# Optimization experiments

Measured on AMD Instinct MI355X. Metric: run time of the kernel, lower is better.

## Reference

```python
import jax, jax.numpy as jnp
import numpy as np

K = 2048  # num_embeddings
D = 64    # embedding_dim


def setup_inputs() -> dict:
    key = jax.random.key(0)
    k1, k2 = jax.random.split(key)
    inputs = jax.random.normal(k1, (64, 32, 32, D), dtype=jnp.float32)
    # tf.random_uniform_initializer default: U[0, 1)
    embeddings = jax.random.uniform(k2, (K, D), dtype=jnp.float32)
    return {"inputs": inputs, "embeddings": embeddings}


def reference(inputs, embeddings):
    input_shape = inputs.shape
    flat_inputs = inputs.reshape(-1, D)  # [N, D]
    distances = (
        jnp.sum(flat_inputs ** 2, axis=1, keepdims=True)
        - 2.0 * jnp.matmul(flat_inputs, embeddings.T)
        + jnp.sum(embeddings ** 2, axis=1)
    )
    encoding_indices = jnp.argmin(distances, axis=1)  # [N]
    quantized = embeddings[encoding_indices].reshape(input_shape)
    # straight-through estimator
    quantized = inputs + jax.lax.stop_gradient(quantized - inputs)
    return quantized, encoding_indices, flat_inputs
```

## Files before the change

### kernel.cpp

```cpp
#include <hip/hip_runtime.h>
#include <cfloat>

#define N_TOTAL 65536
#define DIM     64
#define NEMB    2048

typedef __attribute__((ext_vector_type(8))) _Float16 half8;
typedef __attribute__((ext_vector_type(4))) float    floatx4;

__global__ void prep_kernel(const float* __restrict__ emb,
                            half8* __restrict__ ehp, float* __restrict__ en) {
    const int t = blockIdx.x * 256 + threadIdx.x;
    {
        const int l   = t & 63;
        const int ks  = (t >> 6) & 1;
        const int g   = t >> 7;
        const int col = g * 16 + (l & 15);
        const int kb  = ks * 32 + (l >> 4) * 8;
        const float* s = emb + col * DIM + kb;
        float4 v0 = *(const float4*)s, v1 = *(const float4*)(s + 4);
        half8 hv;
        hv[0] = (_Float16)v0.x; hv[1] = (_Float16)v0.y;
        hv[2] = (_Float16)v0.z; hv[3] = (_Float16)v0.w;
        hv[4] = (_Float16)v1.x; hv[5] = (_Float16)v1.y;
        hv[6] = (_Float16)v1.z; hv[7] = (_Float16)v1.w;
        ehp[t] = hv;
    }
    if (t < NEMB * 4) {
        const int row = t >> 2, seg = t & 3;
        const float* s = emb + row * DIM + seg * 16;
        float acc = 0.f;
#pragma unroll
        for (int i = 0; i < 4; ++i) {
            float4 v = ((const float4*)s)[i];
            acc = fmaf(v.x, v.x, acc); acc = fmaf(v.y, v.y, acc);
            acc = fmaf(v.z, v.z, acc); acc = fmaf(v.w, v.w, acc);
        }
        acc += __shfl_xor(acc, 1, 64);
        acc += __shfl_xor(acc, 2, 64);
        if (seg == 0) en[row] = acc;
    }
}

__global__ __launch_bounds__(256, 4) void vq_mfma_kernel(
        const float* __restrict__ x, const float* __restrict__ emb,
        const char* __restrict__ ehb, const float* __restrict__ eng,
        float* __restrict__ quant, float* __restrict__ idxf,
        float* __restrict__ flat) {

    __shared__ float EnS[NEMB];
    __shared__ uint4 Mrg[2][64];

    const int t    = threadIdx.x;
    const int wave = t >> 6, lane = t & 63;
    const int n = lane & 15, q = lane >> 4;
    const int h = wave & 1, p = wave >> 1;
    const int blk0 = blockIdx.x * 64;
    const int row0 = blk0 + p * 32;

    {
        const float4* s4 = (const float4*)(x + (size_t)blk0 * DIM);
        float4*       d4 = (float4*)(flat + (size_t)blk0 * DIM);
#pragma unroll
        for (int i = 0; i < 4; ++i) d4[i * 256 + t] = s4[i * 256 + t];
    }
    {
        const float4* s4 = (const float4*)eng;
        float4*       d4 = (float4*)EnS;
#pragma unroll
        for (int i = 0; i < 2; ++i) d4[i * 256 + t] = s4[i * 256 + t];
    }

    half8 ah[2][2], al[2][2];
#pragma unroll
    for (int tl = 0; tl < 2; ++tl)
#pragma unroll
        for (int ks = 0; ks < 2; ++ks) {
            const float* pp = x + (size_t)(row0 + tl * 16 + n) * DIM + ks * 32 + q * 8;
            float4 v0 = *(const float4*)pp, v1 = *(const float4*)(pp + 4);
            float xv[8] = {v0.x, v0.y, v0.z, v0.w, v1.x, v1.y, v1.z, v1.w};
#pragma unroll
            for (int j = 0; j < 8; ++j) {
                _Float16 hh = (_Float16)xv[j];
                ah[tl][ks][j] = hh;
                al[tl][ks][j] = (_Float16)(xv[j] - (float)hh);
            }
        }

    __syncthreads();

    unsigned best[8], sec[8];
#pragma unroll
    for (int r = 0; r < 8; ++r) { best[r] = 0u; sec[r] = 0u; }

    const char* ebase = ehb + (size_t)h * 131072 + (size_t)lane * 16;

    half8 bbuf[2][4];
    float enc[2][2];
#pragma unroll
    for (int i = 0; i < 4; ++i)
        bbuf[0][i] = *(const half8*)(ebase + i * 1024);
#pragma unroll
    for (int s = 0; s < 2; ++s)
        enc[0][s] = EnS[h * 1024 + s * 16 + n];

#pragma unroll 2
    for (int tile = 0; tile < 32; ++tile) {
        const int buf = tile & 1;
        if (tile < 31) {
            const char* src = ebase + (size_t)(tile + 1) * 4096;
#pragma unroll
            for (int i = 0; i < 4; ++i)
                bbuf[buf ^ 1][i] = *(const half8*)(src + i * 1024);
#pragma unroll
            for (int s = 0; s < 2; ++s)
                enc[buf ^ 1][s] = EnS[h * 1024 + (tile + 1) * 32 + s * 16 + n];
        }

#pragma unroll
        for (int sub = 0; sub < 2; ++sub) {
            const int L = tile * 2 + sub;
            const float enh = fmaf(-0.5f, enc[buf][sub], 128.0f);
            floatx4 a0 = {enh, enh, enh, enh};
            floatx4 a1 = a0;
            half8 bk0 = bbuf[buf][sub * 2 + 0];
            half8 bk1 = bbuf[buf][sub * 2 + 1];
            a0 = __builtin_amdgcn_mfma_f32_16x16x32_f16(ah[0][0], bk0, a0, 0, 0, 0);
            a1 = __builtin_amdgcn_mfma_f32_16x16x32_f16(ah[1][0], bk0, a1, 0, 0, 0);
            a0 = __builtin_amdgcn_mfma_f32_16x16x32_f16(al[0][0], bk0, a0, 0, 0, 0);
            a1 = __builtin_amdgcn_mfma_f32_16x16x32_f16(al[1][0], bk0, a1, 0, 0, 0);
            a0 = __builtin_amdgcn_mfma_f32_16x16x32_f16(ah[0][1], bk1, a0, 0, 0, 0);
            a1 = __builtin_amdgcn_mfma_f32_16x16x32_f16(ah[1][1], bk1, a1, 0, 0, 0);
            a0 = __builtin_amdgcn_mfma_f32_16x16x32_f16(al[0][1], bk1, a0, 0, 0, 0);
            a1 = __builtin_amdgcn_mfma_f32_16x16x32_f16(al[1][1], bk1, a1, 0, 0, 0);

            const unsigned Lp = (unsigned)(63 - L);
#pragma unroll
            for (int r = 0; r < 8; ++r) {
                float v = (r < 4) ? a0[r] : a1[r - 4];
                unsigned key = (__float_as_uint(v) & 0xFFFFFFC0u) | Lp;
                unsigned lo  = best[r] < key ? best[r] : key;
                best[r] = best[r] > key ? best[r] : key;
                sec[r]  = sec[r] > lo ? sec[r] : lo;
            }
        }
    }

    unsigned bval[8], bcol[8], sval[8], scol[8];
#pragma unroll
    for (int r = 0; r < 8; ++r) {
        bval[r] = best[r] & 0xFFFFFFC0u;
        bcol[r] = (unsigned)(h * 1024 + (63 - (int)(best[r] & 63u)) * 16 + n);
        sval[r] = sec[r] & 0xFFFFFFC0u;
        scol[r] = (unsigned)(h * 1024 + (63 - (int)(sec[r] & 63u)) * 16 + n);
    }
#pragma unroll
    for (int m = 1; m < 16; m <<= 1) {
#pragma unroll
        for (int r = 0; r < 8; ++r) {
            unsigned ov  = (unsigned)__shfl_xor((int)bval[r], m, 64);
            unsigned oc  = (unsigned)__shfl_xor((int)bcol[r], m, 64);
            unsigned ov2 = (unsigned)__shfl_xor((int)sval[r], m, 64);
            unsigned oc2 = (unsigned)__shfl_xor((int)scol[r], m, 64);
            bool ow = (ov > bval[r]) || (ov == bval[r] && oc < bcol[r]);
            unsigned nbv = ow ? ov : bval[r], nbc = ow ? oc : bcol[r];
            unsigned lv  = ow ? bval[r] : ov, lc  = ow ? bcol[r] : oc;
            bool sv2 = (ov2 > sval[r]) || (ov2 == sval[r] && oc2 < scol[r]);
            unsigned bsv = sv2 ? ov2 : sval[r], bsc = sv2 ? oc2 : scol[r];
            bool s3 = (lv > bsv) || (lv == bsv && lc < bsc);
            sval[r] = s3 ? lv : bsv; scol[r] = s3 ? lc : bsc;
            bval[r] = nbv; bcol[r] = nbc;
        }
    }
    if (n == 0) {
#pragma unroll
        for (int r = 0; r < 8; ++r) {
            const int lr = p * 32 + (r >> 2) * 16 + q * 4 + (r & 3);
            Mrg[h][lr] = make_uint4(bval[r], bcol[r], sval[r], scol[r]);
        }
    }
    __syncthreads();

#pragma unroll
    for (int r = 0; r < 4; ++r) {
        const int lr   = wave * 16 + q * 4 + r;
        const int grow = blk0 + lr;
        uint4 c0v = Mrg[0][lr], c1v = Mrg[1][lr];
        int cand[4] = {(int)c0v.y, (int)c0v.w, (int)c1v.y, (int)c1v.w};
        float4 xv = *(const float4*)(x + (size_t)grow * DIM + n * 4);
        float pbest = -FLT_MAX; int cbest = 0;
        float4 ebest = {0.f, 0.f, 0.f, 0.f};
#pragma unroll
        for (int c = 0; c < 4; ++c) {
            float4 e = *(const float4*)(emb + (size_t)cand[c] * DIM + n * 4);
            float pp = (xv.x - 0.5f * e.x) * e.x + (xv.y - 0.5f * e.y) * e.y
                     + (xv.z - 0.5f * e.z) * e.z + (xv.w - 0.5f * e.w) * e.w;
#pragma unroll
            for (int m2 = 1; m2 < 16; m2 <<= 1) pp += __shfl_xor(pp, m2, 64);
            bool take = (pp > pbest) || (pp == pbest && cand[c] < cbest);
            pbest = take ? pp : pbest;
            cbest = take ? cand[c] : cbest;
            ebest.x = take ? e.x : ebest.x; ebest.y = take ? e.y : ebest.y;
            ebest.z = take ? e.z : ebest.z; ebest.w = take ? e.w : ebest.w;
        }
        *(float4*)(quant + (size_t)grow * DIM + n * 4) = ebest;
        if (n == 0) idxf[grow] = (float)cbest;
    }
}

extern "C" void kernel_launch(void* const* d_in, const int* in_sizes, int n_in,
                              void* d_out, int out_size, void* d_ws, size_t ws_size,
                              hipStream_t stream) {
    const float* x   = (const float*)d_in[0];
    const float* emb = (const float*)d_in[1];
    float* out   = (float*)d_out;
    float* quant = out;
    float* idxf  = out + (size_t)N_TOTAL * DIM;
    float* flat  = idxf + N_TOTAL;

    half8* ehp = (half8*)d_ws;
    float* en  = (float*)((char*)d_ws + (size_t)NEMB * DIM * 2);

    prep_kernel<<<64, 256, 0, stream>>>(emb, ehp, en);
    vq_mfma_kernel<<<N_TOTAL / 64, 256, 0, stream>>>(x, emb, (const char*)ehp, en,
                                                     quant, idxf, flat);
}
```

Before: 121.8 us.

## Drop fp16 low-part split, quarter codebook per wave, rescore eight candidates

```diff
diff --git a/kernel.cpp b/kernel.cpp
--- a/kernel.cpp
+++ b/kernel.cpp
@@ -7,6 +7,9 @@
 
 typedef __attribute__((ext_vector_type(8))) _Float16 half8;
 typedef __attribute__((ext_vector_type(4))) float    floatx4;
+
+__device__ __forceinline__ unsigned umin2(unsigned a, unsigned b) { return a < b ? a : b; }
+__device__ __forceinline__ unsigned umax2(unsigned a, unsigned b) { return a > b ? a : b; }
 
 __global__ void prep_kernel(const float* __restrict__ emb,
                             half8* __restrict__ ehp, float* __restrict__ en) {
@@ -38,31 +41,29 @@
         }
         acc += __shfl_xor(acc, 1, 64);
         acc += __shfl_xor(acc, 2, 64);
-        if (seg == 0) en[row] = acc;
+        if (seg == 0) en[row] = fmaf(-0.5f, acc, 128.0f);
     }
 }
 
-__global__ __launch_bounds__(256, 4) void vq_mfma_kernel(
+__global__ __launch_bounds__(256, 6) void vq_mfma_kernel(
         const float* __restrict__ x, const float* __restrict__ emb,
         const char* __restrict__ ehb, const float* __restrict__ eng,
         float* __restrict__ quant, float* __restrict__ idxf,
         float* __restrict__ flat) {
 
     __shared__ float EnS[NEMB];
-    __shared__ uint4 Mrg[2][64];
+    __shared__ uint4 Mrg[4][32];
 
     const int t    = threadIdx.x;
-    const int wave = t >> 6, lane = t & 63;
+    const int h    = t >> 6, lane = t & 63;
     const int n = lane & 15, q = lane >> 4;
-    const int h = wave & 1, p = wave >> 1;
-    const int blk0 = blockIdx.x * 64;
-    const int row0 = blk0 + p * 32;
+    const int blk0 = blockIdx.x * 32;
 
     {
         const float4* s4 = (const float4*)(x + (size_t)blk0 * DIM);
         float4*       d4 = (float4*)(flat + (size_t)blk0 * DIM);
 #pragma unroll
-        for (int i = 0; i < 4; ++i) d4[i * 256 + t] = s4[i * 256 + t];
+        for (int i = 0; i < 2; ++i) d4[i * 256 + t] = s4[i * 256 + t];
     }
     {
         const float4* s4 = (const float4*)eng;
@@ -71,20 +72,17 @@
         for (int i = 0; i < 2; ++i) d4[i * 256 + t] = s4[i * 256 + t];
     }
 
-    half8 ah[2][2], al[2][2];
+    half8 ah[2][2];
 #pragma unroll
     for (int tl = 0; tl < 2; ++tl)
 #pragma unroll
         for (int ks = 0; ks < 2; ++ks) {
-            const float* pp = x + (size_t)(row0 + tl * 16 + n) * DIM + ks * 32 + q * 8;
+            const float* pp = x + (size_t)(blk0 + tl * 16 + n) * DIM + ks * 32 + q * 8;
             float4 v0 = *(const float4*)pp, v1 = *(const float4*)(pp + 4);
-            float xv[8] = {v0.x, v0.y, v0.z, v0.w, v1.x, v1.y, v1.z, v1.w};
-#pragma unroll
-            for (int j = 0; j < 8; ++j) {
-                _Float16 hh = (_Float16)xv[j];
-                ah[tl][ks][j] = hh;
-                al[tl][ks][j] = (_Float16)(xv[j] - (float)hh);
-            }
+            ah[tl][ks][0] = (_Float16)v0.x; ah[tl][ks][1] = (_Float16)v0.y;
+            ah[tl][ks][2] = (_Float16)v0.z; ah[tl][ks][3] = (_Float16)v0.w;
+            ah[tl][ks][4] = (_Float16)v1.x; ah[tl][ks][5] = (_Float16)v1.y;
+            ah[tl][ks][6] = (_Float16)v1.z; ah[tl][ks][7] = (_Float16)v1.w;
         }
 
     __syncthreads();
@@ -93,7 +91,7 @@
 #pragma unroll
     for (int r = 0; r < 8; ++r) { best[r] = 0u; sec[r] = 0u; }
 
-    const char* ebase = ehb + (size_t)h * 131072 + (size_t)lane * 16;
+    const char* ebase = ehb + (size_t)h * 65536 + (size_t)lane * 16;
 
     half8 bbuf[2][4];
     float enc[2][2];
@@ -102,47 +100,49 @@
         bbuf[0][i] = *(const half8*)(ebase + i * 1024);
 #pragma unroll
     for (int s = 0; s < 2; ++s)
-        enc[0][s] = EnS[h * 1024 + s * 16 + n];
+        enc[0][s] = EnS[h * 512 + s * 16 + n];
 
 #pragma unroll 2
-    for (int tile = 0; tile < 32; ++tile) {
+    for (int tile = 0; tile < 16; ++tile) {
         const int buf = tile & 1;
-        if (tile < 31) {
+        if (tile < 15) {
             const char* src = ebase + (size_t)(tile + 1) * 4096;
 #pragma unroll
             for (int i = 0; i < 4; ++i)
                 bbuf[buf ^ 1][i] = *(const half8*)(src + i * 1024);
 #pragma unroll
             for (int s = 0; s < 2; ++s)
-                enc[buf ^ 1][s] = EnS[h * 1024 + (tile + 1) * 32 + s * 16 + n];
-        }
-
-#pragma unroll
-        for (int sub = 0; sub < 2; ++sub) {
-            const int L = tile * 2 + sub;
-            const float enh = fmaf(-0.5f, enc[buf][sub], 128.0f);
-            floatx4 a0 = {enh, enh, enh, enh};
-            floatx4 a1 = a0;
-            half8 bk0 = bbuf[buf][sub * 2 + 0];
-            half8 bk1 = bbuf[buf][sub * 2 + 1];
-            a0 = __builtin_amdgcn_mfma_f32_16x16x32_f16(ah[0][0], bk0, a0, 0, 0, 0);
-            a1 = __builtin_amdgcn_mfma_f32_16x16x32_f16(ah[1][0], bk0, a1, 0, 0, 0);
-            a0 = __builtin_amdgcn_mfma_f32_16x16x32_f16(al[0][0], bk0, a0, 0, 0, 0);
-            a1 = __builtin_amdgcn_mfma_f32_16x16x32_f16(al[1][0], bk0, a1, 0, 0, 0);
-            a0 = __builtin_amdgcn_mfma_f32_16x16x32_f16(ah[0][1], bk1, a0, 0, 0, 0);
-            a1 = __builtin_amdgcn_mfma_f32_16x16x32_f16(ah[1][1], bk1, a1, 0, 0, 0);
-            a0 = __builtin_amdgcn_mfma_f32_16x16x32_f16(al[0][1], bk1, a0, 0, 0, 0);
-            a1 = __builtin_amdgcn_mfma_f32_16x16x32_f16(al[1][1], bk1, a1, 0, 0, 0);
-
-            const unsigned Lp = (unsigned)(63 - L);
-#pragma unroll
-            for (int r = 0; r < 8; ++r) {
-                float v = (r < 4) ? a0[r] : a1[r - 4];
-                unsigned key = (__float_as_uint(v) & 0xFFFFFFC0u) | Lp;
-                unsigned lo  = best[r] < key ? best[r] : key;
-                best[r] = best[r] > key ? best[r] : key;
-                sec[r]  = sec[r] > lo ? sec[r] : lo;
-            }
+                enc[buf ^ 1][s] = EnS[h * 512 + (tile + 1) * 32 + s * 16 + n];
+        }
+
+        const float e0 = enc[buf][0], e1 = enc[buf][1];
+        floatx4 A0 = {e0, e0, e0, e0};
+        floatx4 A1 = {e0, e0, e0, e0};
+        floatx4 A2 = {e1, e1, e1, e1};
+        floatx4 A3 = {e1, e1, e1, e1};
+        A0 = __builtin_amdgcn_mfma_f32_16x16x32_f16(ah[0][0], bbuf[buf][0], A0, 0, 0, 0);
+        A1 = __builtin_amdgcn_mfma_f32_16x16x32_f16(ah[1][0], bbuf[buf][0], A1, 0, 0, 0);
+        A2 = __builtin_amdgcn_mfma_f32_16x16x32_f16(ah[0][0], bbuf[buf][2], A2, 0, 0, 0);
+        A3 = __builtin_amdgcn_mfma_f32_16x16x32_f16(ah[1][0], bbuf[buf][2], A3, 0, 0, 0);
+        A0 = __builtin_amdgcn_mfma_f32_16x16x32_f16(ah[0][1], bbuf[buf][1], A0, 0, 0, 0);
+        A1 = __builtin_amdgcn_mfma_f32_16x16x32_f16(ah[1][1], bbuf[buf][1], A1, 0, 0, 0);
+        A2 = __builtin_amdgcn_mfma_f32_16x16x32_f16(ah[0][1], bbuf[buf][3], A2, 0, 0, 0);
+        A3 = __builtin_amdgcn_mfma_f32_16x16x32_f16(ah[1][1], bbuf[buf][3], A3, 0, 0, 0);
+
+        const unsigned Lp0 = (unsigned)(63 - (tile * 2 + 0));
+        const unsigned Lp1 = (unsigned)(63 - (tile * 2 + 1));
+#pragma unroll
+        for (int r = 0; r < 8; ++r) {
+            float v0 = (r < 4) ? A0[r] : A1[r - 4];
+            unsigned k0 = (__float_as_uint(v0) & 0xFFFFFFC0u) | Lp0;
+            unsigned lo0 = umin2(best[r], k0);
+            best[r] = umax2(best[r], k0);
+            sec[r]  = umax2(sec[r], lo0);
+            float v1 = (r < 4) ? A2[r] : A3[r - 4];
+            unsigned k1 = (__float_as_uint(v1) & 0xFFFFFFC0u) | Lp1;
+            unsigned lo1 = umin2(best[r], k1);
+            best[r] = umax2(best[r], k1);
+            sec[r]  = umax2(sec[r], lo1);
         }
     }
 
@@ -150,9 +150,9 @@
 #pragma unroll
     for (int r = 0; r < 8; ++r) {
         bval[r] = best[r] & 0xFFFFFFC0u;
-        bcol[r] = (unsigned)(h * 1024 + (63 - (int)(best[r] & 63u)) * 16 + n);
+        bcol[r] = (unsigned)(h * 512 + (63 - (int)(best[r] & 63u)) * 16 + n);
         sval[r] = sec[r] & 0xFFFFFFC0u;
-        scol[r] = (unsigned)(h * 1024 + (63 - (int)(sec[r] & 63u)) * 16 + n);
+        scol[r] = (unsigned)(h * 512 + (63 - (int)(sec[r] & 63u)) * 16 + n);
     }
 #pragma unroll
     for (int m = 1; m < 16; m <<= 1) {
@@ -175,23 +175,28 @@
     if (n == 0) {
 #pragma unroll
         for (int r = 0; r < 8; ++r) {
-            const int lr = p * 32 + (r >> 2) * 16 + q * 4 + (r & 3);
+            const int lr = (r >> 2) * 16 + q * 4 + (r & 3);
             Mrg[h][lr] = make_uint4(bval[r], bcol[r], sval[r], scol[r]);
         }
     }
     __syncthreads();
 
 #pragma unroll
-    for (int r = 0; r < 4; ++r) {
-        const int lr   = wave * 16 + q * 4 + r;
+    for (int rr = 0; rr < 2; ++rr) {
+        const int lr   = h * 8 + q * 2 + rr;
         const int grow = blk0 + lr;
-        uint4 c0v = Mrg[0][lr], c1v = Mrg[1][lr];
-        int cand[4] = {(int)c0v.y, (int)c0v.w, (int)c1v.y, (int)c1v.w};
+        int cand[8];
+#pragma unroll
+        for (int g = 0; g < 4; ++g) {
+            uint4 cv = Mrg[g][lr];
+            cand[g * 2 + 0] = (int)cv.y;
+            cand[g * 2 + 1] = (int)cv.w;
+        }
         float4 xv = *(const float4*)(x + (size_t)grow * DIM + n * 4);
         float pbest = -FLT_MAX; int cbest = 0;
         float4 ebest = {0.f, 0.f, 0.f, 0.f};
 #pragma unroll
-        for (int c = 0; c < 4; ++c) {
+        for (int c = 0; c < 8; ++c) {
             float4 e = *(const float4*)(emb + (size_t)cand[c] * DIM + n * 4);
             float pp = (xv.x - 0.5f * e.x) * e.x + (xv.y - 0.5f * e.y) * e.y
                      + (xv.z - 0.5f * e.z) * e.z + (xv.w - 0.5f * e.w) * e.w;
@@ -222,6 +227,6 @@
     float* en  = (float*)((char*)d_ws + (size_t)NEMB * DIM * 2);
 
     prep_kernel<<<64, 256, 0, stream>>>(emb, ehp, en);
-    vq_mfma_kernel<<<N_TOTAL / 64, 256, 0, stream>>>(x, emb, (const char*)ehp, en,
+    vq_mfma_kernel<<<N_TOTAL / 32, 256, 0, stream>>>(x, emb, (const char*)ehp, en,
                                                      quant, idxf, flat);
 }
```

New measurement: 243.1 us. +99.6%, slower.
